# Optimization experiments

Hardware: AMD Instinct MI355X
Metric: run time of the kernel (lower is better)

The kernel has to match this reference:

```python
import jax, jax.numpy as jnp
import numpy as np

H = 16
D = 1024
DH = D // H


def setup_inputs() -> dict:
    key = jax.random.key(0)
    ks = jax.random.split(key, 7)
    B, N = 4, 2048
    queries = jax.random.normal(ks[0], (B, N, D), dtype=jnp.float32)
    keys = jax.random.normal(ks[1], (B, N, D), dtype=jnp.float32)
    values = jax.random.normal(ks[2], (B, N, D), dtype=jnp.float32)
    s = 1.0 / np.sqrt(D)
    Wq = jax.random.normal(ks[3], (D, D), dtype=jnp.float32) * s
    Wk = jax.random.normal(ks[4], (D, D), dtype=jnp.float32) * s
    Wv = jax.random.normal(ks[5], (D, D), dtype=jnp.float32) * s
    Wo = jax.random.normal(ks[6], (D, D), dtype=jnp.float32) * s
    return {"queries": queries, "keys": keys, "values": values,
            "Wq": Wq, "Wk": Wk, "Wv": Wv, "Wo": Wo}


def reference(queries, keys, values, Wq, Wk, Wv, Wo):
    B, Nq, _ = queries.shape
    Nk = keys.shape[1]
    # torch Linear (no bias): y = x @ W.T
    q = (queries @ Wq.T).reshape(B, Nq, H, DH)
    k = (keys @ Wk.T).reshape(B, Nk, H, DH)
    v = (values @ Wv.T).reshape(B, Nk, H, DH)
    scale = 1.0 / jnp.sqrt(jnp.asarray(DH, dtype=q.dtype))
    scores = jnp.einsum("bqhd,bkhd->bhqk", q, k) * scale  # (B,H,Nq,Nk)
    attn = jax.nn.softmax(scores, axis=-1)
    ctx = jnp.einsum("bhqk,bkhd->bqhd", attn, v).reshape(B, Nq, D)
    return ctx @ Wo.T
```

## Files before the change

kernel.cpp:

```cpp
#include <hip/hip_runtime.h>
#include <hip/hip_bf16.h>
#include <stdint.h>

typedef short bf16x8 __attribute__((ext_vector_type(8)));
typedef float f32x4 __attribute__((ext_vector_type(4)));
typedef unsigned short u16;
typedef unsigned int u32;

#define MFMA(a, b, c) __builtin_amdgcn_mfma_f32_16x16x32_bf16(a, b, c, 0, 0, 0)

#if __has_builtin(__builtin_amdgcn_exp2f)
#define EXP2F(x) __builtin_amdgcn_exp2f(x)
#else
#define EXP2F(x) exp2f(x)
#endif
#if __has_builtin(__builtin_amdgcn_rcpf)
#define RCPF(x) __builtin_amdgcn_rcpf(x)
#else
#define RCPF(x) (1.0f / (x))
#endif

__device__ __forceinline__ u16 f2bf(float f) {
  u32 u = __builtin_bit_cast(u32, f);
  u += 0x7FFFu + ((u >> 16) & 1u);
  return (u16)(u >> 16);
}

__device__ __forceinline__ bf16x8 cvt8(const float* p) {
  const float4 f0 = *(const float4*)p;
  const float4 f1 = *(const float4*)(p + 4);
  bf16x8 r;
  r[0] = (short)f2bf(f0.x); r[1] = (short)f2bf(f0.y);
  r[2] = (short)f2bf(f0.z); r[3] = (short)f2bf(f0.w);
  r[4] = (short)f2bf(f1.x); r[5] = (short)f2bf(f1.y);
  r[6] = (short)f2bf(f1.z); r[7] = (short)f2bf(f1.w);
  return r;
}

__device__ __forceinline__ void async16(const u16* g, u16* l) {
  __builtin_amdgcn_global_load_lds(
      (const __attribute__((address_space(1))) void*)g,
      (__attribute__((address_space(3))) void*)l, 16, 0, 0);
}

__global__ __launch_bounds__(256) void cvt_qk(const float* __restrict__ xq,
                                              const float* __restrict__ xk,
                                              u16* __restrict__ dq,
                                              u16* __restrict__ dk) {
  int b = (int)blockIdx.x;
  const float* s;
  u16* d;
  if (b < 4096) { s = xq; d = dq; } else { s = xk; d = dk; b -= 4096; }
  const size_t off = (size_t)b * 2048 + (size_t)threadIdx.x * 8;
  *(bf16x8*)(d + off) = cvt8(s + off);
}

__global__ __launch_bounds__(256) void cvt_vw(
    const float* __restrict__ xv, const float* __restrict__ wq,
    const float* __restrict__ wk, const float* __restrict__ wv,
    const float* __restrict__ wo, u16* __restrict__ dv, u16* __restrict__ dwq,
    u16* __restrict__ dwk, u16* __restrict__ dwv, u16* __restrict__ dwo) {
  int b = (int)blockIdx.x;
  const float* s;
  u16* d;
  if (b < 4096) { s = xv; d = dv; }
  else if (b < 4608) { s = wq; d = dwq; b -= 4096; }
  else if (b < 5120) { s = wk; d = dwk; b -= 4608; }
  else if (b < 5632) { s = wv; d = dwv; b -= 5120; }
  else { s = wo; d = dwo; b -= 5632; }
  const size_t off = (size_t)b * 2048 + (size_t)threadIdx.x * 8;
  *(bf16x8*)(d + off) = cvt8(s + off);
}

template <int MODE, typename OutT>
__global__ __launch_bounds__(256, 2) void gemm_bt(const u16* __restrict__ A,
                                                  const u16* __restrict__ W,
                                                  OutT* __restrict__ out) {
  __shared__ u16 smA[128 * 64];
  __shared__ u16 smB[128 * 64];
  const int tid = (int)threadIdx.x;
  const int w = tid >> 6, l = tid & 63;
  const int la = l & 15, q = l >> 4;
  const int m0 = blockIdx.x * 128, n0 = blockIdx.y * 128;
  const int wm = w >> 1, wn = w & 1;

  const int srow = tid >> 3, sblk = tid & 7;
  f32x4 acc[4][4];
#pragma unroll
  for (int i = 0; i < 4; ++i)
#pragma unroll
    for (int j = 0; j < 4; ++j) acc[i][j] = (f32x4){0.f, 0.f, 0.f, 0.f};

  for (int kk = 0; kk < 16; ++kk) {
    __syncthreads();
#pragma unroll
    for (int jj = 0; jj < 4; ++jj) {
      const int row = jj * 32 + srow;
      const int sb = (sblk ^ (row & 7)) * 8;
      const int ld = (jj * 256 + tid) * 8;
      async16(A + (size_t)(m0 + row) * 1024 + kk * 64 + sb, smA + ld);
      async16(W + (size_t)(n0 + row) * 1024 + kk * 64 + sb, smB + ld);
    }
    __syncthreads();
#pragma unroll
    for (int ks = 0; ks < 2; ++ks) {
      bf16x8 af[4], bfr[4];
#pragma unroll
      for (int im = 0; im < 4; ++im)
        af[im] = *(const bf16x8*)(smA + (wm * 64 + im * 16 + la) * 64 +
                                  (((ks * 4 + q) ^ (la & 7)) * 8));
#pragma unroll
      for (int in = 0; in < 4; ++in)
        bfr[in] = *(const bf16x8*)(smB + (wn * 64 + in * 16 + la) * 64 +
                                   (((ks * 4 + q) ^ (la & 7)) * 8));
#pragma unroll
      for (int im = 0; im < 4; ++im)
#pragma unroll
        for (int in = 0; in < 4; ++in)
          acc[im][in] = MFMA(af[im], bfr[in], acc[im][in]);
    }
  }

#pragma unroll
  for (int im = 0; im < 4; ++im) {
    const int mbase = m0 + wm * 64 + im * 16 + q * 4;
#pragma unroll
    for (int in = 0; in < 4; ++in) {
      const int n = n0 + wn * 64 + in * 16 + la;
      if (MODE == 2) {
        const int b = mbase >> 11, nr = mbase & 2047;
        const int h = n >> 6, d = n & 63;
        uint2 val;
        val.x = (u32)f2bf(acc[im][in][0]) | ((u32)f2bf(acc[im][in][1]) << 16);
        val.y = (u32)f2bf(acc[im][in][2]) | ((u32)f2bf(acc[im][in][3]) << 16);
        *(uint2*)((u16*)out + ((size_t)((b * 16 + h) * 64 + d)) * 2048 + nr) = val;
      } else if (MODE == 0) {
#pragma unroll
        for (int r = 0; r < 4; ++r) {
          const int mm = mbase + r;
          ((float*)out)[(size_t)mm * 1024 + n] = acc[im][in][r];
        }
      } else {
#pragma unroll
        for (int r = 0; r < 4; ++r) {
          const int mm = mbase + r;
          const int b = mm >> 11, nr = mm & 2047;
          const int h = n >> 6, d = n & 63;
          ((u16*)out)[((size_t)((b * 16 + h) * 2048 + nr)) * 64 + d] = f2bf(acc[im][in][r]);
        }
      }
    }
  }
}

__global__ __launch_bounds__(256, 2) void attn_kernel(const u16* __restrict__ Qh,
                                                      const u16* __restrict__ Kh,
                                                      const u16* __restrict__ VT,
                                                      u16* __restrict__ ctx) {
  __shared__ u16 smK[128 * 64];
  __shared__ u16 smV[64 * 128];
  __shared__ u16 smP[128 * 128];

  const int tid = (int)threadIdx.x;
  const int w = tid >> 6, l = tid & 63;
  const int la = l & 15, q = l >> 4;
  const int qt = blockIdx.x, bh = blockIdx.y;
  const u16* Qp = Qh + (size_t)bh * (2048 * 64);
  const u16* Kp = Kh + (size_t)bh * (2048 * 64);
  const u16* Vp = VT + (size_t)bh * (64 * 2048);

  bf16x8 qf[2][2];
#pragma unroll
  for (int ic = 0; ic < 2; ++ic)
#pragma unroll
    for (int ks = 0; ks < 2; ++ks)
      qf[ic][ks] = *(const bf16x8*)(Qp + (size_t)(qt * 128 + w * 32 + ic * 16 + la) * 64 +
                                    ks * 32 + q * 8);

  f32x4 accO[2][4];
#pragma unroll
  for (int ic = 0; ic < 2; ++ic)
#pragma unroll
    for (int dc = 0; dc < 4; ++dc) accO[ic][dc] = (f32x4){0.f, 0.f, 0.f, 0.f};
  float m_[2] = {-__builtin_inff(), -__builtin_inff()};
  float l_[2] = {0.f, 0.f};
  float alpha_[2];
  const float SC = 0.18033688011112042f;

  for (int kt = 0; kt < 16; ++kt) {
    __syncthreads();
#pragma unroll
    for (int jj = 0; jj < 4; ++jj) {
      const int idx = jj * 256 + tid;
      const int kr = idx >> 3, kb = idx & 7;
      const bf16x8 vk = *(const bf16x8*)(Kp + (size_t)(kt * 128 + kr) * 64 + kb * 8);
      *(bf16x8*)(smK + kr * 64 + ((kb ^ (kr & 7)) * 8)) = vk;
      const int vr = idx >> 4, vb = idx & 15;
      const bf16x8 vv = *(const bf16x8*)(Vp + (size_t)vr * 2048 + kt * 128 + vb * 8);
      *(bf16x8*)(smV + vr * 128 + ((vb ^ (vr & 15)) * 8)) = vv;
    }
    __syncthreads();

    f32x4 st[2][8];
#pragma unroll
    for (int ic = 0; ic < 2; ++ic)
#pragma unroll
      for (int jc = 0; jc < 8; ++jc) st[ic][jc] = (f32x4){0.f, 0.f, 0.f, 0.f};
#pragma unroll
    for (int ks = 0; ks < 2; ++ks) {
      bf16x8 kf[8];
#pragma unroll
      for (int jc = 0; jc < 8; ++jc)
        kf[jc] = *(const bf16x8*)(smK + (jc * 16 + la) * 64 +
                                  (((ks * 4 + q) ^ (la & 7)) * 8));
#pragma unroll
      for (int jc = 0; jc < 8; ++jc)
#pragma unroll
        for (int ic = 0; ic < 2; ++ic)
          st[ic][jc] = MFMA(kf[jc], qf[ic][ks], st[ic][jc]);
    }

#pragma unroll
    for (int ic = 0; ic < 2; ++ic) {
      float mx = -__builtin_inff();
#pragma unroll
      for (int jc = 0; jc < 8; ++jc)
#pragma unroll
        for (int r = 0; r < 4; ++r) {
          const float t = st[ic][jc][r] * SC;
          st[ic][jc][r] = t;
          mx = fmaxf(mx, t);
        }
      mx = fmaxf(mx, __shfl_xor(mx, 16));
      mx = fmaxf(mx, __shfl_xor(mx, 32));
      const float mnew = fmaxf(m_[ic], mx);
      alpha_[ic] = EXP2F(m_[ic] - mnew);
      float rs = 0.f;
      const int i = w * 32 + ic * 16 + la;
#pragma unroll
      for (int jc = 0; jc < 8; ++jc) {
        const float p0 = EXP2F(st[ic][jc][0] - mnew);
        const float p1 = EXP2F(st[ic][jc][1] - mnew);
        const float p2 = EXP2F(st[ic][jc][2] - mnew);
        const float p3 = EXP2F(st[ic][jc][3] - mnew);
        rs += (p0 + p1) + (p2 + p3);
        uint2 val;
        val.x = (u32)f2bf(p0) | ((u32)f2bf(p1) << 16);
        val.y = (u32)f2bf(p2) | ((u32)f2bf(p3) << 16);
        const int blk = (jc * 2 + (q >> 1)) ^ la;
        *(uint2*)(smP + i * 128 + blk * 8 + (q & 1) * 4) = val;
      }
      rs += __shfl_xor(rs, 16);
      rs += __shfl_xor(rs, 32);
      m_[ic] = mnew;
      l_[ic] = l_[ic] * alpha_[ic] + rs;
    }
    __syncthreads();

#pragma unroll
    for (int ic = 0; ic < 2; ++ic)
#pragma unroll
      for (int r = 0; r < 4; ++r) {
        const float a = __shfl(alpha_[ic], q * 4 + r);
#pragma unroll
        for (int dc = 0; dc < 4; ++dc) accO[ic][dc][r] *= a;
      }

#pragma unroll
    for (int ks = 0; ks < 4; ++ks) {
      bf16x8 pf[2], vf[4];
#pragma unroll
      for (int ic = 0; ic < 2; ++ic)
        pf[ic] = *(const bf16x8*)(smP + (w * 32 + ic * 16 + la) * 128 +
                                  (((ks * 4 + q) ^ la) * 8));
#pragma unroll
      for (int dc = 0; dc < 4; ++dc)
        vf[dc] = *(const bf16x8*)(smV + (dc * 16 + la) * 128 +
                                  (((ks * 4 + q) ^ la) * 8));
#pragma unroll
      for (int ic = 0; ic < 2; ++ic)
#pragma unroll
        for (int dc = 0; dc < 4; ++dc)
          accO[ic][dc] = MFMA(pf[ic], vf[dc], accO[ic][dc]);
    }
  }

  const int b = bh >> 4, h = bh & 15;
#pragma unroll
  for (int ic = 0; ic < 2; ++ic)
#pragma unroll
    for (int r = 0; r < 4; ++r) {
      const float inv = RCPF(__shfl(l_[ic], q * 4 + r));
      const size_t rowoff =
          ((size_t)(b * 2048 + qt * 128 + w * 32 + ic * 16 + q * 4 + r)) * 1024 + h * 64;
#pragma unroll
      for (int dc = 0; dc < 4; ++dc)
        ctx[rowoff + dc * 16 + la] = f2bf(accO[ic][dc][r] * inv);
    }
}

extern "C" void kernel_launch(void* const* d_in, const int* in_sizes, int n_in,
                              void* d_out, int out_size, void* d_ws, size_t ws_size,
                              hipStream_t stream) {
  const float* Xq = (const float*)d_in[0];
  const float* Xk = (const float*)d_in[1];
  const float* Xv = (const float*)d_in[2];
  const float* Wq = (const float*)d_in[3];
  const float* Wk = (const float*)d_in[4];
  const float* Wv = (const float*)d_in[5];
  const float* Wo = (const float*)d_in[6];

  const size_t T = 8388608;
  const size_t WN = 1048576;
  u16 *Xqb, *Xkb, *Xvb, *Wqb, *Wkb, *Wvb, *Wob, *Qh, *Kh, *VTp, *ctx;
  if (ws_size >= (7 * T + 4 * WN) * sizeof(u16)) {
    u16* ws = (u16*)d_ws;
    Xqb = ws; Xkb = ws + T; Xvb = ws + 2 * T;
    Qh = ws + 3 * T; Kh = ws + 4 * T; VTp = ws + 5 * T; ctx = ws + 6 * T;
    Wqb = ws + 7 * T; Wkb = Wqb + WN; Wvb = Wkb + WN; Wob = Wvb + WN;
  } else {
    u16* ob = (u16*)d_out;
    u16* bq = (u16*)d_in[0];
    u16* bk = (u16*)d_in[1];
    u16* bv = (u16*)d_in[2];
    Xqb = ob; Xkb = ob + T;
    Xvb = bq; Wqb = bq + T; Wkb = Wqb + WN; Wvb = Wkb + WN; Wob = Wvb + WN;
    Qh = bk; Kh = bk + T;
    VTp = bv; ctx = bv + T;
  }

  dim3 blk(256);
  hipLaunchKernelGGL(cvt_qk, dim3(8192), blk, 0, stream, Xq, Xk, Xqb, Xkb);
  hipLaunchKernelGGL(cvt_vw, dim3(6144), blk, 0, stream, Xv, Wq, Wk, Wv, Wo,
                     Xvb, Wqb, Wkb, Wvb, Wob);
  dim3 gg(64, 8);
  hipLaunchKernelGGL((gemm_bt<1, u16>), gg, blk, 0, stream, Xqb, Wqb, Qh);
  hipLaunchKernelGGL((gemm_bt<1, u16>), gg, blk, 0, stream, Xkb, Wkb, Kh);
  hipLaunchKernelGGL((gemm_bt<2, u16>), gg, blk, 0, stream, Xvb, Wvb, VTp);
  hipLaunchKernelGGL(attn_kernel, dim3(16, 64), blk, 0, stream, Qh, Kh, VTp, ctx);
  hipLaunchKernelGGL((gemm_bt<0, float>), gg, blk, 0, stream, ctx, Wob, (float*)d_out);
}
```

Before: 372.8 us.

## Merge QKV GEMMs, fold softmax scale into Q, lazy rescale, read V from global

New measurement: 481.8 us. 1.29x slower.

```diff
diff --git a/kernel.cpp b/kernel.cpp
--- a/kernel.cpp
+++ b/kernel.cpp
@@ -72,10 +72,103 @@
   *(bf16x8*)(d + off) = cvt8(s + off);
 }
 
-template <int MODE, typename OutT>
-__global__ __launch_bounds__(256, 2) void gemm_bt(const u16* __restrict__ A,
-                                                  const u16* __restrict__ W,
-                                                  OutT* __restrict__ out) {
+__device__ __forceinline__ void gemm_core(const u16* __restrict__ A,
+                                          const u16* __restrict__ W,
+                                          u16* smA, u16* smB, f32x4 acc[4][4],
+                                          int m0, int n0, int tid) {
+  const int w = tid >> 6, l = tid & 63;
+  const int la = l & 15, q = l >> 4;
+  const int wm = w >> 1, wn = w & 1;
+  const int srow = tid >> 3, sblk = tid & 7;
+
+  for (int kk = 0; kk < 16; ++kk) {
+    __syncthreads();
+#pragma unroll
+    for (int jj = 0; jj < 4; ++jj) {
+      const int row = jj * 32 + srow;
+      const int sb = (sblk ^ (row & 7)) * 8;
+      const int ld = (jj * 256 + tid) * 8;
+      async16(A + (size_t)(m0 + row) * 1024 + kk * 64 + sb, smA + ld);
+      async16(W + (size_t)(n0 + row) * 1024 + kk * 64 + sb, smB + ld);
+    }
+    __syncthreads();
+#pragma unroll
+    for (int ks = 0; ks < 2; ++ks) {
+      bf16x8 af[4], bfr[4];
+#pragma unroll
+      for (int im = 0; im < 4; ++im)
+        af[im] = *(const bf16x8*)(smA + (wm * 64 + im * 16 + la) * 64 +
+                                  (((ks * 4 + q) ^ (la & 7)) * 8));
+#pragma unroll
+      for (int in = 0; in < 4; ++in)
+        bfr[in] = *(const bf16x8*)(smB + (wn * 64 + in * 16 + la) * 64 +
+                                   (((ks * 4 + q) ^ (la & 7)) * 8));
+#pragma unroll
+      for (int im = 0; im < 4; ++im)
+#pragma unroll
+        for (int in = 0; in < 4; ++in)
+          acc[im][in] = MFMA(af[im], bfr[in], acc[im][in]);
+    }
+  }
+}
+
+__global__ __launch_bounds__(256, 3) void gemm_qkv(
+    const u16* __restrict__ Xqb, const u16* __restrict__ Xkb,
+    const u16* __restrict__ Xvb, const u16* __restrict__ Wqb,
+    const u16* __restrict__ Wkb, const u16* __restrict__ Wvb,
+    u16* __restrict__ Qh, u16* __restrict__ Kh, u16* __restrict__ VTp) {
+  __shared__ u16 smA[128 * 64];
+  __shared__ u16 smB[128 * 64];
+  const int z = (int)blockIdx.z;
+  const u16* A = (z == 0) ? Xqb : (z == 1) ? Xkb : Xvb;
+  const u16* W = (z == 0) ? Wqb : (z == 1) ? Wkb : Wvb;
+  u16* out = (z == 0) ? Qh : (z == 1) ? Kh : VTp;
+  const float scale = (z == 0) ? 0.18033688011112042f : 1.0f;
+
+  const int tid = (int)threadIdx.x;
+  const int w = tid >> 6, l = tid & 63;
+  const int la = l & 15, q = l >> 4;
+  const int m0 = blockIdx.x * 128, n0 = blockIdx.y * 128;
+  const int wm = w >> 1, wn = w & 1;
+
+  f32x4 acc[4][4];
+#pragma unroll
+  for (int i = 0; i < 4; ++i)
+#pragma unroll
+    for (int j = 0; j < 4; ++j) acc[i][j] = (f32x4){0.f, 0.f, 0.f, 0.f};
+
+  gemm_core(A, W, smA, smB, acc, m0, n0, tid);
+
+#pragma unroll
+  for (int im = 0; im < 4; ++im) {
+    const int mbase = m0 + wm * 64 + im * 16 + q * 4;
+#pragma unroll
+    for (int in = 0; in < 4; ++in) {
+      const int n = n0 + wn * 64 + in * 16 + la;
+      if (z == 2) {
+        const int b = mbase >> 11, nr = mbase & 2047;
+        const int h = n >> 6, d = n & 63;
+        uint2 val;
+        val.x = (u32)f2bf(acc[im][in][0]) | ((u32)f2bf(acc[im][in][1]) << 16);
+        val.y = (u32)f2bf(acc[im][in][2]) | ((u32)f2bf(acc[im][in][3]) << 16);
+        *(uint2*)(VTp + ((size_t)((b * 16 + h) * 64 + d)) * 2048 + nr) = val;
+      } else {
+#pragma unroll
+        for (int r = 0; r < 4; ++r) {
+          const int mm = mbase + r;
+          const int b = mm >> 11, nr = mm & 2047;
+          const int h = n >> 6, d = n & 63;
+          out[((size_t)((b * 16 + h) * 2048 + nr)) * 64 + d] =
+              f2bf(acc[im][in][r] * scale);
+        }
+      }
+    }
+  }
+}
+
+__global__ __launch_bounds__(256, 3) void gemm_out(const u16* __restrict__ A,
+                                                   const u16* __restrict__ W,
+                                                   float* __restrict__ out) {
   __shared__ u16 smA[128 * 64];
   __shared__ u16 smB[128 * 64];
   const int tid = (int)threadIdx.x;
@@ -84,42 +177,13 @@
   const int m0 = blockIdx.x * 128, n0 = blockIdx.y * 128;
   const int wm = w >> 1, wn = w & 1;
 
-  const int srow = tid >> 3, sblk = tid & 7;
   f32x4 acc[4][4];
 #pragma unroll
   for (int i = 0; i < 4; ++i)
 #pragma unroll
     for (int j = 0; j < 4; ++j) acc[i][j] = (f32x4){0.f, 0.f, 0.f, 0.f};
 
-  for (int kk = 0; kk < 16; ++kk) {
-    __syncthreads();
-#pragma unroll
-    for (int jj = 0; jj < 4; ++jj) {
-      const int row = jj * 32 + srow;
-      const int sb = (sblk ^ (row & 7)) * 8;
-      const int ld = (jj * 256 + tid) * 8;
-      async16(A + (size_t)(m0 + row) * 1024 + kk * 64 + sb, smA + ld);
-      async16(W + (size_t)(n0 + row) * 1024 + kk * 64 + sb, smB + ld);
-    }
-    __syncthreads();
-#pragma unroll
-    for (int ks = 0; ks < 2; ++ks) {
-      bf16x8 af[4], bfr[4];
-#pragma unroll
-      for (int im = 0; im < 4; ++im)
-        af[im] = *(const bf16x8*)(smA + (wm * 64 + im * 16 + la) * 64 +
-                                  (((ks * 4 + q) ^ (la & 7)) * 8));
-#pragma unroll
-      for (int in = 0; in < 4; ++in)
-        bfr[in] = *(const bf16x8*)(smB + (wn * 64 + in * 16 + la) * 64 +
-                                   (((ks * 4 + q) ^ (la & 7)) * 8));
-#pragma unroll
-      for (int im = 0; im < 4; ++im)
-#pragma unroll
-        for (int in = 0; in < 4; ++in)
-          acc[im][in] = MFMA(af[im], bfr[in], acc[im][in]);
-    }
-  }
+  gemm_core(A, W, smA, smB, acc, m0, n0, tid);
 
 #pragma unroll
   for (int im = 0; im < 4; ++im) {
@@ -127,38 +191,18 @@
 #pragma unroll
     for (int in = 0; in < 4; ++in) {
       const int n = n0 + wn * 64 + in * 16 + la;
-      if (MODE == 2) {
-        const int b = mbase >> 11, nr = mbase & 2047;
-        const int h = n >> 6, d = n & 63;
-        uint2 val;
-        val.x = (u32)f2bf(acc[im][in][0]) | ((u32)f2bf(acc[im][in][1]) << 16);
-        val.y = (u32)f2bf(acc[im][in][2]) | ((u32)f2bf(acc[im][in][3]) << 16);
-        *(uint2*)((u16*)out + ((size_t)((b * 16 + h) * 64 + d)) * 2048 + nr) = val;
-      } else if (MODE == 0) {
-#pragma unroll
-        for (int r = 0; r < 4; ++r) {
-          const int mm = mbase + r;
-          ((float*)out)[(size_t)mm * 1024 + n] = acc[im][in][r];
-        }
-      } else {
-#pragma unroll
-        for (int r = 0; r < 4; ++r) {
-          const int mm = mbase + r;
-          const int b = mm >> 11, nr = mm & 2047;
-          const int h = n >> 6, d = n & 63;
-          ((u16*)out)[((size_t)((b * 16 + h) * 2048 + nr)) * 64 + d] = f2bf(acc[im][in][r]);
-        }
-      }
-    }
-  }
-}
-
-__global__ __launch_bounds__(256, 2) void attn_kernel(const u16* __restrict__ Qh,
+#pragma unroll
+      for (int r = 0; r < 4; ++r)
+        out[(size_t)(mbase + r) * 1024 + n] = acc[im][in][r];
+    }
+  }
+}
+
+__global__ __launch_bounds__(256, 3) void attn_kernel(const u16* __restrict__ Qh,
                                                       const u16* __restrict__ Kh,
                                                       const u16* __restrict__ VT,
                                                       u16* __restrict__ ctx) {
   __shared__ u16 smK[128 * 64];
-  __shared__ u16 smV[64 * 128];
   __shared__ u16 smP[128 * 128];
 
   const int tid = (int)threadIdx.x;
@@ -185,19 +229,17 @@
   float m_[2] = {-__builtin_inff(), -__builtin_inff()};
   float l_[2] = {0.f, 0.f};
   float alpha_[2];
-  const float SC = 0.18033688011112042f;
+  bool skip_[2];
+
+  const int srow = tid >> 3, sblk = tid & 7;
 
   for (int kt = 0; kt < 16; ++kt) {
     __syncthreads();
 #pragma unroll
     for (int jj = 0; jj < 4; ++jj) {
-      const int idx = jj * 256 + tid;
-      const int kr = idx >> 3, kb = idx & 7;
-      const bf16x8 vk = *(const bf16x8*)(Kp + (size_t)(kt * 128 + kr) * 64 + kb * 8);
-      *(bf16x8*)(smK + kr * 64 + ((kb ^ (kr & 7)) * 8)) = vk;
-      const int vr = idx >> 4, vb = idx & 15;
-      const bf16x8 vv = *(const bf16x8*)(Vp + (size_t)vr * 2048 + kt * 128 + vb * 8);
-      *(bf16x8*)(smV + vr * 128 + ((vb ^ (vr & 15)) * 8)) = vv;
+      const int row = jj * 32 + srow;
+      const int sb = (sblk ^ (row & 7)) * 8;
+      async16(Kp + (size_t)(kt * 128 + row) * 64 + sb, smK + (jj * 256 + tid) * 8);
     }
     __syncthreads();
 
@@ -206,6 +248,7 @@
     for (int ic = 0; ic < 2; ++ic)
 #pragma unroll
       for (int jc = 0; jc < 8; ++jc) st[ic][jc] = (f32x4){0.f, 0.f, 0.f, 0.f};
+    __builtin_amdgcn_s_setprio(1);
 #pragma unroll
     for (int ks = 0; ks < 2; ++ks) {
       bf16x8 kf[8];
@@ -219,6 +262,7 @@
         for (int ic = 0; ic < 2; ++ic)
           st[ic][jc] = MFMA(kf[jc], qf[ic][ks], st[ic][jc]);
     }
+    __builtin_amdgcn_s_setprio(0);
 
 #pragma unroll
     for (int ic = 0; ic < 2; ++ic) {
@@ -226,15 +270,15 @@
 #pragma unroll
       for (int jc = 0; jc < 8; ++jc)
 #pragma unroll
-        for (int r = 0; r < 4; ++r) {
-          const float t = st[ic][jc][r] * SC;
-          st[ic][jc][r] = t;
-          mx = fmaxf(mx, t);
-        }
+        for (int r = 0; r < 4; ++r) mx = fmaxf(mx, st[ic][jc][r]);
       mx = fmaxf(mx, __shfl_xor(mx, 16));
       mx = fmaxf(mx, __shfl_xor(mx, 32));
-      const float mnew = fmaxf(m_[ic], mx);
-      alpha_[ic] = EXP2F(m_[ic] - mnew);
+      const bool skip = (bool)__all(mx - m_[ic] <= 8.0f);
+      float mnew, al;
+      if (skip) { mnew = m_[ic]; al = 1.0f; }
+      else { mnew = fmaxf(m_[ic], mx); al = EXP2F(m_[ic] - mnew); }
+      skip_[ic] = skip;
+      alpha_[ic] = al;
       float rs = 0.f;
       const int i = w * 32 + ic * 16 + la;
 #pragma unroll
@@ -259,11 +303,13 @@
 
 #pragma unroll
     for (int ic = 0; ic < 2; ++ic)
-#pragma unroll
-      for (int r = 0; r < 4; ++r) {
-        const float a = __shfl(alpha_[ic], q * 4 + r);
-#pragma unroll
-        for (int dc = 0; dc < 4; ++dc) accO[ic][dc][r] *= a;
+      if (!skip_[ic]) {
+#pragma unroll
+        for (int r = 0; r < 4; ++r) {
+          const float a = __shfl(alpha_[ic], q * 4 + r);
+#pragma unroll
+          for (int dc = 0; dc < 4; ++dc) accO[ic][dc][r] *= a;
+        }
       }
 
 #pragma unroll
@@ -275,13 +321,15 @@
                                   (((ks * 4 + q) ^ la) * 8));
 #pragma unroll
       for (int dc = 0; dc < 4; ++dc)
-        vf[dc] = *(const bf16x8*)(smV + (dc * 16 + la) * 128 +
-                                  (((ks * 4 + q) ^ la) * 8));
+        vf[dc] = *(const bf16x8*)(Vp + (size_t)(dc * 16 + la) * 2048 +
+                                  kt * 128 + ks * 32 + q * 8);
+      __builtin_amdgcn_s_setprio(1);
 #pragma unroll
       for (int ic = 0; ic < 2; ++ic)
 #pragma unroll
         for (int dc = 0; dc < 4; ++dc)
           accO[ic][dc] = MFMA(pf[ic], vf[dc], accO[ic][dc]);
+      __builtin_amdgcn_s_setprio(0);
     }
   }
 
@@ -333,10 +381,8 @@
   hipLaunchKernelGGL(cvt_qk, dim3(8192), blk, 0, stream, Xq, Xk, Xqb, Xkb);
   hipLaunchKernelGGL(cvt_vw, dim3(6144), blk, 0, stream, Xv, Wq, Wk, Wv, Wo,
                      Xvb, Wqb, Wkb, Wvb, Wob);
-  dim3 gg(64, 8);
-  hipLaunchKernelGGL((gemm_bt<1, u16>), gg, blk, 0, stream, Xqb, Wqb, Qh);
-  hipLaunchKernelGGL((gemm_bt<1, u16>), gg, blk, 0, stream, Xkb, Wkb, Kh);
-  hipLaunchKernelGGL((gemm_bt<2, u16>), gg, blk, 0, stream, Xvb, Wvb, VTp);
+  hipLaunchKernelGGL(gemm_qkv, dim3(64, 8, 3), blk, 0, stream, Xqb, Xkb, Xvb,
+                     Wqb, Wkb, Wvb, Qh, Kh, VTp);
   hipLaunchKernelGGL(attn_kernel, dim3(16, 64), blk, 0, stream, Qh, Kh, VTp, ctx);
-  hipLaunchKernelGGL((gemm_bt<0, float>), gg, blk, 0, stream, ctx, Wob, (float*)d_out);
-}
+  hipLaunchKernelGGL(gemm_out, dim3(64, 8), blk, 0, stream, ctx, Wob, (float*)d_out);
+}
```
